# Performance work log

Measured on AMD Instinct MI355X. Metric: run time of the kernel, lower is better.

## Reference

```python
import jax, jax.numpy as jnp
import numpy as np

N_NODES = 50000
N_EDGES = 800000
NODE_DIM = 128
EDGE_DIM = 32
HIDDEN = 128
OUT_DIM = 128


def _linear_params(key, fan_in, fan_out):
    k1, k2 = jax.random.split(key)
    bound = 1.0 / np.sqrt(fan_in)
    W = jax.random.uniform(k1, (fan_in, fan_out), minval=-bound, maxval=bound, dtype=jnp.float32)
    b = jax.random.uniform(k2, (fan_out,), minval=-bound, maxval=bound, dtype=jnp.float32)
    return W, b


def setup_inputs() -> dict:
    key = jax.random.key(0)
    ks = jax.random.split(key, 7)
    h = jax.random.normal(ks[0], (N_NODES, NODE_DIM), dtype=jnp.float32)
    edge_index = jax.random.randint(ks[1], (2, N_EDGES), 0, N_NODES, dtype=jnp.int64)
    edge_attr = jax.random.normal(ks[2], (N_EDGES, EDGE_DIM), dtype=jnp.float32)
    We1, be1 = _linear_params(ks[3], 2 * NODE_DIM + EDGE_DIM, HIDDEN)
    We2, be2 = _linear_params(ks[4], HIDDEN, HIDDEN)
    Wh1, bh1 = _linear_params(ks[5], NODE_DIM + HIDDEN, HIDDEN)
    Wh2, bh2 = _linear_params(ks[6], HIDDEN, OUT_DIM)
    return {"h": h, "edge_index": edge_index, "edge_attr": edge_attr,
            "We1": We1, "be1": be1, "We2": We2, "be2": be2,
            "Wh1": Wh1, "bh1": bh1, "Wh2": Wh2, "bh2": bh2}


def _mlp(x, W1, b1, W2, b2):
    return jax.nn.relu(x @ W1 + b1) @ W2 + b2


def reference(h, edge_index, edge_attr, We1, be1, We2, be2, Wh1, bh1, Wh2, bh2):
    src = edge_index[0]
    dst = edge_index[1]
    # gather endpoint features and concat with edge attributes: [E, 2*D+De]
    edge_input = jnp.concatenate([h[src], h[dst], edge_attr], axis=-1)
    m_ij = _mlp(edge_input, We1, be1, We2, be2)  # [E, H]
    # scatter-add messages into destination nodes
    m_i = jax.ops.segment_sum(m_ij, dst, num_segments=h.shape[0])  # [N, H]
    node_input = jnp.concatenate([h, m_i], axis=-1)  # [N, D+H]
    h_next = _mlp(node_input, Wh1, bh1, Wh2, bh2)  # [N, out]
    return h_next
```

## Files before the change

### kernel.cpp

```cpp
#include <hip/hip_runtime.h>

#define E_TOTAL 800000
#define N_TOTAL 50000
#define NBINS   50176

typedef __attribute__((ext_vector_type(8))) short short8;
typedef __attribute__((ext_vector_type(4))) float floatx4;

__device__ __forceinline__ unsigned short f2bf(float f) {
    union { float f; unsigned u; } x; x.f = f;
    unsigned r = x.u + 0x7fff + ((x.u >> 16) & 1);
    return (unsigned short)(r >> 16);
}

__device__ __forceinline__ void gload_lds16(const void* g, void* l) {
    __builtin_amdgcn_global_load_lds(
        (const __attribute__((address_space(1))) void*)g,
        (__attribute__((address_space(3))) void*)l, 16, 0, 0);
}
__device__ __forceinline__ void gload_lds4(const void* g, void* l) {
    __builtin_amdgcn_global_load_lds(
        (const __attribute__((address_space(1))) void*)g,
        (__attribute__((address_space(3))) void*)l, 4, 0, 0);
}

__global__ __launch_bounds__(256)
void prep(const float* __restrict__ We1, const float* __restrict__ We2,
          const float* __restrict__ Wh1, const float* __restrict__ Wh2,
          unsigned short* __restrict__ W1t, unsigned short* __restrict__ W2t,
          unsigned short* __restrict__ Wh1t, unsigned short* __restrict__ Wh2t,
          const float* __restrict__ h, unsigned short* __restrict__ hbf,
          int do_cvt, int do_sort,
          float* __restrict__ mi, int* __restrict__ hist)
{
    const int b = blockIdx.x;
    const int tid = threadIdx.x;
    if (b < 400) {
        int t = b * 256 + tid;
        if (t < 36864) {
            W1t[(t & 127) * 288 + (t >> 7)] = f2bf(We1[t]);
        } else if (t < 53248) {
            t -= 36864;
            W2t[(t & 127) * 128 + (t >> 7)] = f2bf(We2[t]);
        } else if (t < 86016) {
            t -= 53248;
            Wh1t[(t & 127) * 256 + (t >> 7)] = f2bf(Wh1[t]);
        } else if (t < 102400) {
            t -= 86016;
            Wh2t[(t & 127) * 128 + (t >> 7)] = f2bf(Wh2[t]);
        }
    } else if (b < 6650) {
        const int t = (b - 400) * 256 + tid;
        ((float4*)mi)[t] = make_float4(0.f, 0.f, 0.f, 0.f);
    } else if (b < 9775) {
        if (do_cvt) {
            const int t = (b - 6650) * 256 + tid;
            const float4* h4 = (const float4*)h;
            float4 a = h4[(size_t)t * 2];
            float4 c = h4[(size_t)t * 2 + 1];
            short8 v = { (short)f2bf(a.x), (short)f2bf(a.y), (short)f2bf(a.z), (short)f2bf(a.w),
                         (short)f2bf(c.x), (short)f2bf(c.y), (short)f2bf(c.z), (short)f2bf(c.w) };
            *(short8*)(&hbf[(size_t)t * 8]) = v;
        }
    } else {
        if (do_sort) hist[(b - 9775) * 256 + tid] = 0;
    }
}

__global__ __launch_bounds__(256) void k_hist(const int* __restrict__ ei, int* __restrict__ hist) {
    const int t = blockIdx.x * 256 + threadIdx.x;
    atomicAdd(&hist[ei[E_TOTAL + t]], 1);
}
__global__ __launch_bounds__(256) void k_scan1(const int* __restrict__ hist, int* __restrict__ partial) {
    __shared__ int s[256];
    s[threadIdx.x] = hist[blockIdx.x * 256 + threadIdx.x];
    __syncthreads();
    for (int off = 128; off > 0; off >>= 1) {
        if (threadIdx.x < off) s[threadIdx.x] += s[threadIdx.x + off];
        __syncthreads();
    }
    if (threadIdx.x == 0) partial[blockIdx.x] = s[0];
}
__global__ __launch_bounds__(256)
void k_scan2(const int* __restrict__ partial, int* __restrict__ partialOff) {
    __shared__ int s[256];
    const int t = threadIdx.x;
    const int NP = NBINS / 256;
    const int v = (t < NP) ? partial[t] : 0;
    s[t] = v; __syncthreads();
    for (int off = 1; off < 256; off <<= 1) {
        int x = (t >= off) ? s[t - off] : 0;
        __syncthreads();
        s[t] += x;
        __syncthreads();
    }
    if (t < NP) partialOff[t] = s[t] - v;
}
__global__ __launch_bounds__(256)
void k_scan3(const int* __restrict__ hist, const int* __restrict__ partialOff,
             int* __restrict__ cursor) {
    __shared__ int s[256];
    const int t = threadIdx.x, g = blockIdx.x * 256 + t;
    const int v = hist[g];
    s[t] = v; __syncthreads();
    for (int off = 1; off < 256; off <<= 1) {
        int x = (t >= off) ? s[t - off] : 0;
        __syncthreads();
        s[t] += x;
        __syncthreads();
    }
    cursor[g] = partialOff[blockIdx.x] + s[t] - v;
}
__global__ __launch_bounds__(256)
void k_scatter(const int* __restrict__ ei, const float* __restrict__ ea,
               int* __restrict__ cursor,
               int* __restrict__ srcS, int* __restrict__ dstS,
               unsigned short* __restrict__ eabf) {
    const int t = blockIdx.x * 256 + threadIdx.x;
    const int src = ei[t];
    const int dst = ei[E_TOTAL + t];
    const int pos = atomicAdd(&cursor[dst], 1);
    srcS[pos] = src;
    dstS[pos] = dst;
    const float4* ea4 = (const float4*)ea;
    #pragma unroll
    for (int j = 0; j < 4; ++j) {
        float4 a = ea4[(size_t)t * 8 + j * 2];
        float4 b = ea4[(size_t)t * 8 + j * 2 + 1];
        short8 v = { (short)f2bf(a.x), (short)f2bf(a.y), (short)f2bf(a.z), (short)f2bf(a.w),
                     (short)f2bf(b.x), (short)f2bf(b.y), (short)f2bf(b.z), (short)f2bf(b.w) };
        *(short8*)(&eabf[(size_t)pos * 32 + j * 8]) = v;
    }
}

constexpr int XK = 296;
constexpr int HK = 136;
constexpr int NK = 264;
constexpr int FJ = 132;

#define MFMA8(A, B, C) { \
    C[0][0] = __builtin_amdgcn_mfma_f32_16x16x32_bf16(A[0], B[0], C[0][0], 0, 0, 0); \
    C[0][1] = __builtin_amdgcn_mfma_f32_16x16x32_bf16(A[0], B[1], C[0][1], 0, 0, 0); \
    C[1][0] = __builtin_amdgcn_mfma_f32_16x16x32_bf16(A[1], B[0], C[1][0], 0, 0, 0); \
    C[1][1] = __builtin_amdgcn_mfma_f32_16x16x32_bf16(A[1], B[1], C[1][1], 0, 0, 0); \
    C[2][0] = __builtin_amdgcn_mfma_f32_16x16x32_bf16(A[2], B[0], C[2][0], 0, 0, 0); \
    C[2][1] = __builtin_amdgcn_mfma_f32_16x16x32_bf16(A[2], B[1], C[2][1], 0, 0, 0); \
    C[3][0] = __builtin_amdgcn_mfma_f32_16x16x32_bf16(A[3], B[0], C[3][0], 0, 0, 0); \
    C[3][1] = __builtin_amdgcn_mfma_f32_16x16x32_bf16(A[3], B[1], C[3][1], 0, 0, 0); }

__global__ __launch_bounds__(256, 2)
void edge_mfma_sorted(const unsigned short* __restrict__ hbf,
                      const int* __restrict__ srcS,
                      const int* __restrict__ dstS,
                      const unsigned short* __restrict__ eabf,
                      const unsigned short* __restrict__ W1t,
                      const float* __restrict__ b1,
                      const unsigned short* __restrict__ W2t,
                      const float* __restrict__ b2,
                      float* __restrict__ mi)
{
    constexpr int NT = E_TOTAL / 64;
    constexpr int XH = 64 * 288;
    __shared__ alignas(16) unsigned short sMem[2 * XH + 768];
    int* idb = (int*)&sMem[2 * XH];

    const int tid  = threadIdx.x;
    const int lane = tid & 63;
    const int w    = tid >> 6;
    const int q    = lane >> 4;
    const int lr   = lane & 15;
    const int n0   = w * 32;
    const int q8   = q * 8;
    const int S    = (int)gridDim.x;

    const int w1b0 = (n0 + lr) * 288, w1b1 = (n0 + 16 + lr) * 288;
    const int w2b0 = (n0 + lr) * 128, w2b1 = (n0 + 16 + lr) * 128;
    const int h0 = lr * HK, h1 = (16 + lr) * HK, h2 = (32 + lr) * HK, h3 = (48 + lr) * HK;

    const float bias1[2] = { b1[n0 + lr], b1[n0 + 16 + lr] };
    const float bias2[2] = { b2[n0 + lr], b2[n0 + 16 + lr] };

    auto ID_DMA = [&](int tt, int k) {
        if (w == 0)      gload_lds4(srcS + tt * 64 + lane, &idb[k * 128]);
        else if (w == 1) gload_lds4(dstS + tt * 64 + lane, &idb[k * 128 + 64]);
    };

    auto X_DMA = [&](int tt, int bufS, int k) {
        const int* ids = &idb[k * 128];
        #pragma unroll
        for (int j = 0; j < 9; ++j) {
            const int tj = j * 256 + tid;
            const int e  = tj / 36;
            const int p  = tj - e * 36;
            const int c  = (p < 32) ? (p ^ (e & 15)) : p;
            const int node = ids[((c & 16) ? 64 : 0) + e];
            const char* gh = (const char*)hbf + (size_t)node * 256 + (size_t)(c & 15) * 16;
            const char* ge = (const char*)eabf + ((size_t)tt * 64 + e) * 64 + (size_t)(p - 32) * 16;
            const void* g  = (p < 32) ? (const void*)gh : (const void*)ge;
            gload_lds16(g, (void*)&sMem[bufS + j * 2048 + w * 512]);
        }
    };

#define LA1(KS, A) { \
    const int cs = ((KS) < 8) ? ((((KS) * 4 + q) ^ lr) * 8) : ((32 + q) * 8); \
    A[0] = *(const short8*)(&sX[( 0 + lr) * 288 + cs]); \
    A[1] = *(const short8*)(&sX[(16 + lr) * 288 + cs]); \
    A[2] = *(const short8*)(&sX[(32 + lr) * 288 + cs]); \
    A[3] = *(const short8*)(&sX[(48 + lr) * 288 + cs]); }
#define LB1(KS, B) { B[0] = *(const short8*)(&W1t[w1b0 + (KS) * 32 + q8]); \
                     B[1] = *(const short8*)(&W1t[w1b1 + (KS) * 32 + q8]); }
#define LA2(KS, A) { A[0] = *(const short8*)(&sX[h0 + (KS) * 32 + q8]); \
                     A[1] = *(const short8*)(&sX[h1 + (KS) * 32 + q8]); \
                     A[2] = *(const short8*)(&sX[h2 + (KS) * 32 + q8]); \
                     A[3] = *(const short8*)(&sX[h3 + (KS) * 32 + q8]); }
#define LB2(KS, B) { B[0] = *(const short8*)(&W2t[w2b0 + (KS) * 32 + q8]); \
                     B[1] = *(const short8*)(&W2t[w2b1 + (KS) * 32 + q8]); }

    int t  = blockIdx.x;
    int cur = 0, ib = 0;

    ID_DMA(t, 0);
    ID_DMA(t + S, 1);
    __syncthreads();
    X_DMA(t, 0, 0);
    __syncthreads();

    while (t < NT) {
        unsigned short* sX = &sMem[cur * XH];

        const int t2 = t + 2 * S;
        if (t2 < NT) ID_DMA(t2, (ib + 2) % 3);
        const int tn = t + S;
        if (tn < NT) X_DMA(tn, (cur ^ 1) * XH, (ib + 1) % 3);

        floatx4 acc[4][2];
        #pragma unroll
        for (int mt = 0; mt < 4; ++mt)
            #pragma unroll
            for (int nt = 0; nt < 2; ++nt)
                acc[mt][nt] = (floatx4){0.f, 0.f, 0.f, 0.f};
        {
            short8 aX[4], aY[4], bX[2], bY[2];
            LB1(0, bX); LB1(1, bY); LA1(0, aX);
            LA1(1, aY); MFMA8(aX, bX, acc); LB1(2, bX);
            LA1(2, aX); MFMA8(aY, bY, acc); LB1(3, bY);
            LA1(3, aY); MFMA8(aX, bX, acc); LB1(4, bX);
            LA1(4, aX); MFMA8(aY, bY, acc); LB1(5, bY);
            LA1(5, aY); MFMA8(aX, bX, acc); LB1(6, bX);
            LA1(6, aX); MFMA8(aY, bY, acc); LB1(7, bY);
            LA1(7, aY); MFMA8(aX, bX, acc); LB1(8, bX);
            LA1(8, aX); MFMA8(aY, bY, acc);
            MFMA8(aX, bX, acc);
        }
        __syncthreads();

        {
            #pragma unroll
            for (int mt = 0; mt < 4; ++mt)
                #pragma unroll
                for (int nt = 0; nt < 2; ++nt)
                    #pragma unroll
                    for (int r = 0; r < 4; ++r) {
                        float v = fmaxf(acc[mt][nt][r] + bias1[nt], 0.f);
                        sX[(mt * 16 + q * 4 + r) * HK + n0 + nt * 16 + lr] = f2bf(v);
                    }
        }
        __syncthreads();

        floatx4 acc2[4][2];
        #pragma unroll
        for (int mt = 0; mt < 4; ++mt)
            #pragma unroll
            for (int nt = 0; nt < 2; ++nt)
                acc2[mt][nt] = (floatx4){0.f, 0.f, 0.f, 0.f};
        {
            short8 aX[4], aY[4], bX[2], bY[2];
            LB2(0, bX); LB2(1, bY); LA2(0, aX);
            LA2(1, aY); MFMA8(aX, bX, acc2); LB2(2, bX);
            LA2(2, aX); MFMA8(aY, bY, acc2); LB2(3, bY);
            LA2(3, aY); MFMA8(aX, bX, acc2);
            MFMA8(aY, bY, acc2);
        }
        __syncthreads();

        float* sF = (float*)sX;
        {
            #pragma unroll
            for (int mt = 0; mt < 4; ++mt)
                #pragma unroll
                for (int nt = 0; nt < 2; ++nt)
                    #pragma unroll
                    for (int r = 0; r < 4; ++r)
                        sF[(mt * 16 + q * 4 + r) * FJ + n0 + nt * 16 + lr] =
                            acc2[mt][nt][r] + bias2[nt];
        }
        __syncthreads();

        {
            const int* idsDst = &idb[ib * 128 + 64];
            const int g  = tid >> 7;
            const int j  = tid & 127;
            const int r0 = g * 32;
            float sum = 0.f;
            for (int r = r0; r < r0 + 32; ++r) {
                sum += sF[r * FJ + j];
                const int dst = idsDst[r];
                if (r == r0 + 31 || idsDst[r + 1] != dst) {
                    atomicAdd(&mi[(size_t)dst * 128 + j], sum);
                    sum = 0.f;
                }
            }
        }
        __syncthreads();

        cur ^= 1;
        ib = (ib == 2) ? 0 : ib + 1;
        t = tn;
    }
#undef LA1
#undef LB1
#undef LA2
#undef LB2
}

template <bool PRECVT>
__global__ __launch_bounds__(256, 8)
void edge_mfma_flat(const float* __restrict__ h,
                    const unsigned short* __restrict__ hbf,
                    const int* __restrict__ ei,
                    const float* __restrict__ ea,
                    const unsigned short* __restrict__ W1t,
                    const float* __restrict__ b1,
                    const unsigned short* __restrict__ W2t,
                    const float* __restrict__ b2,
                    float* __restrict__ mi)
{
    __shared__ unsigned short sMem[32 * XK];
    __shared__ int sDst[32];

    const int tid = threadIdx.x;
    const int e0  = blockIdx.x * 32;
    if (tid < 32) sDst[tid] = ei[E_TOTAL + e0 + tid];

    const float4* h4   = (const float4*)h;
    const short8* hbf8 = (const short8*)hbf;
    const float4* ea4  = (const float4*)ea;
    #pragma unroll
    for (int it = 0; it < 5; ++it) {
        const int idx = tid + it * 256;
        const int e  = idx / 40;
        const int c  = idx - e * 40;
        const int ge = e0 + e;
        if (c < 32) {
            const int node = (c < 16) ? ei[ge] : ei[E_TOTAL + ge];
            const int cc = c & 15;
            short8 v;
            if (PRECVT) {
                v = hbf8[(size_t)node * 16 + cc];
            } else {
                float4 x = h4[(size_t)node * 32 + cc * 2];
                float4 y = h4[(size_t)node * 32 + cc * 2 + 1];
                v = (short8){ (short)f2bf(x.x), (short)f2bf(x.y), (short)f2bf(x.z), (short)f2bf(x.w),
                              (short)f2bf(y.x), (short)f2bf(y.y), (short)f2bf(y.z), (short)f2bf(y.w) };
            }
            *(short8*)(&sMem[e * XK + c * 8]) = v;
        } else {
            float4 x = ea4[(size_t)ge * 8 + (c - 32)];
            unsigned short* p = &sMem[e * XK + 128 + c * 4];
            p[0] = f2bf(x.x); p[1] = f2bf(x.y); p[2] = f2bf(x.z); p[3] = f2bf(x.w);
        }
    }
    __syncthreads();

    const int lane = tid & 63;
    const int w    = tid >> 6;
    const int q    = lane >> 4;
    const int lr   = lane & 15;
    const int n0   = w * 32;

    floatx4 acc[2][2];
    #pragma unroll
    for (int mt = 0; mt < 2; ++mt)
        #pragma unroll
        for (int nt = 0; nt < 2; ++nt)
            acc[mt][nt] = (floatx4){0.f, 0.f, 0.f, 0.f};
    #pragma unroll
    for (int ks = 0; ks < 9; ++ks) {
        const int kb = ks * 32 + q * 8;
        short8 a[2], b[2];
        #pragma unroll
        for (int mt = 0; mt < 2; ++mt)
            a[mt] = *(const short8*)(&sMem[(mt * 16 + lr) * XK + kb]);
        #pragma unroll
        for (int nt = 0; nt < 2; ++nt)
            b[nt] = *(const short8*)(&W1t[(n0 + nt * 16 + lr) * 288 + kb]);
        #pragma unroll
        for (int mt = 0; mt < 2; ++mt)
            #pragma unroll
            for (int nt = 0; nt < 2; ++nt)
                acc[mt][nt] = __builtin_amdgcn_mfma_f32_16x16x32_bf16(
                    a[mt], b[nt], acc[mt][nt], 0, 0, 0);
    }
    __syncthreads();
    {
        float bias[2] = { b1[n0 + lr], b1[n0 + 16 + lr] };
        #pragma unroll
        for (int mt = 0; mt < 2; ++mt)
            #pragma unroll
            for (int nt = 0; nt < 2; ++nt)
                #pragma unroll
                for (int r = 0; r < 4; ++r) {
                    float v = fmaxf(acc[mt][nt][r] + bias[nt], 0.f);
                    sMem[(mt * 16 + q * 4 + r) * HK + n0 + nt * 16 + lr] = f2bf(v);
                }
    }
    __syncthreads();
    floatx4 acc2[2][2];
    #pragma unroll
    for (int mt = 0; mt < 2; ++mt)
        #pragma unroll
        for (int nt = 0; nt < 2; ++nt)
            acc2[mt][nt] = (floatx4){0.f, 0.f, 0.f, 0.f};
    #pragma unroll
    for (int ks = 0; ks < 4; ++ks) {
        const int kb = ks * 32 + q * 8;
        short8 a[2], b[2];
        #pragma unroll
        for (int mt = 0; mt < 2; ++mt)
            a[mt] = *(const short8*)(&sMem[(mt * 16 + lr) * HK + kb]);
        #pragma unroll
        for (int nt = 0; nt < 2; ++nt)
            b[nt] = *(const short8*)(&W2t[(n0 + nt * 16 + lr) * 128 + kb]);
        #pragma unroll
        for (int mt = 0; mt < 2; ++mt)
            #pragma unroll
            for (int nt = 0; nt < 2; ++nt)
                acc2[mt][nt] = __builtin_amdgcn_mfma_f32_16x16x32_bf16(
                    a[mt], b[nt], acc2[mt][nt], 0, 0, 0);
    }
    {
        float bias[2] = { b2[n0 + lr], b2[n0 + 16 + lr] };
        #pragma unroll
        for (int mt = 0; mt < 2; ++mt)
            #pragma unroll
            for (int r = 0; r < 4; ++r) {
                const int m   = mt * 16 + q * 4 + r;
                const int dst = sDst[m];
                float* row = &mi[(size_t)dst * 128];
                #pragma unroll
                for (int nt = 0; nt < 2; ++nt)
                    atomicAdd(&row[n0 + nt * 16 + lr], acc2[mt][nt][r] + bias[nt]);
            }
    }
}

template <bool USEHBF>
__global__ __launch_bounds__(256, 8)
void node_mfma(const float* __restrict__ h,
               const unsigned short* __restrict__ hbf,
               const float* __restrict__ mi,
               const unsigned short* __restrict__ W1t,
               const float* __restrict__ b1,
               const unsigned short* __restrict__ W2t,
               const float* __restrict__ b2,
               float* __restrict__ out)
{
    __shared__ unsigned short sMem[32 * NK];

    const int tid = threadIdx.x;
    const int g0  = blockIdx.x * 32;

    const float4* h4   = (const float4*)h;
    const short8* hbf8 = (const short8*)hbf;
    const float4* mi4  = (const float4*)mi;
    if (USEHBF) {
        #pragma unroll
        for (int it = 0; it < 2; ++it) {
            const int idx = tid + it * 256;
            const int n  = idx >> 4;
            const int c  = idx & 15;
            const int gn = g0 + n;
            short8 v = (short8){0,0,0,0,0,0,0,0};
            if (gn < N_TOTAL) v = hbf8[(size_t)gn * 16 + c];
            *(short8*)(&sMem[n * NK + c * 8]) = v;
        }
        #pragma unroll
        for (int it = 0; it < 4; ++it) {
            const int idx = tid + it * 256;
            const int n  = idx >> 5;
            const int c  = idx & 31;
            const int gn = g0 + n;
            float4 v = make_float4(0.f, 0.f, 0.f, 0.f);
            if (gn < N_TOTAL) v = mi4[(size_t)gn * 32 + c];
            unsigned short* p = &sMem[n * NK + 128 + c * 4];
            p[0] = f2bf(v.x); p[1] = f2bf(v.y); p[2] = f2bf(v.z); p[3] = f2bf(v.w);
        }
    } else {
        #pragma unroll
        for (int it = 0; it < 8; ++it) {
            const int idx = tid + it * 256;
            const int n  = idx >> 6;
            const int c  = idx & 63;
            const int gn = g0 + n;
            float4 v = make_float4(0.f, 0.f, 0.f, 0.f);
            if (gn < N_TOTAL)
                v = (c < 32) ? h4[(size_t)gn * 32 + c] : mi4[(size_t)gn * 32 + (c - 32)];
            unsigned short* p = &sMem[n * NK + c * 4];
            p[0] = f2bf(v.x); p[1] = f2bf(v.y); p[2] = f2bf(v.z); p[3] = f2bf(v.w);
        }
    }
    __syncthreads();

    const int lane = tid & 63;
    const int w    = tid >> 6;
    const int q    = lane >> 4;
    const int lr   = lane & 15;
    const int n0   = w * 32;

    floatx4 acc[2][2];
    #pragma unroll
    for (int mt = 0; mt < 2; ++mt)
        #pragma unroll
        for (int nt = 0; nt < 2; ++nt)
            acc[mt][nt] = (floatx4){0.f, 0.f, 0.f, 0.f};
    #pragma unroll
    for (int ks = 0; ks < 8; ++ks) {
        const int kb = ks * 32 + q * 8;
        short8 a[2], b[2];
        #pragma unroll
        for (int mt = 0; mt < 2; ++mt)
            a[mt] = *(const short8*)(&sMem[(mt * 16 + lr) * NK + kb]);
        #pragma unroll
        for (int nt = 0; nt < 2; ++nt)
            b[nt] = *(const short8*)(&W1t[(n0 + nt * 16 + lr) * 256 + kb]);
        #pragma unroll
        for (int mt = 0; mt < 2; ++mt)
            #pragma unroll
            for (int nt = 0; nt < 2; ++nt)
                acc[mt][nt] = __builtin_amdgcn_mfma_f32_16x16x32_bf16(
                    a[mt], b[nt], acc[mt][nt], 0, 0, 0);
    }
    __syncthreads();
    {
        float bias[2] = { b1[n0 + lr], b1[n0 + 16 + lr] };
        #pragma unroll
        for (int mt = 0; mt < 2; ++mt)
            #pragma unroll
            for (int nt = 0; nt < 2; ++nt)
                #pragma unroll
                for (int r = 0; r < 4; ++r) {
                    float v = fmaxf(acc[mt][nt][r] + bias[nt], 0.f);
                    sMem[(mt * 16 + q * 4 + r) * HK + n0 + nt * 16 + lr] = f2bf(v);
                }
    }
    __syncthreads();
    floatx4 acc2[2][2];
    #pragma unroll
    for (int mt = 0; mt < 2; ++mt)
        #pragma unroll
        for (int nt = 0; nt < 2; ++nt)
            acc2[mt][nt] = (floatx4){0.f, 0.f, 0.f, 0.f};
    #pragma unroll
    for (int ks = 0; ks < 4; ++ks) {
        const int kb = ks * 32 + q * 8;
        short8 a[2], b[2];
        #pragma unroll
        for (int mt = 0; mt < 2; ++mt)
            a[mt] = *(const short8*)(&sMem[(mt * 16 + lr) * HK + kb]);
        #pragma unroll
        for (int nt = 0; nt < 2; ++nt)
            b[nt] = *(const short8*)(&W2t[(n0 + nt * 16 + lr) * 128 + kb]);
        #pragma unroll
        for (int mt = 0; mt < 2; ++mt)
            #pragma unroll
            for (int nt = 0; nt < 2; ++nt)
                acc2[mt][nt] = __builtin_amdgcn_mfma_f32_16x16x32_bf16(
                    a[mt], b[nt], acc2[mt][nt], 0, 0, 0);
    }
    {
        float bias[2] = { b2[n0 + lr], b2[n0 + 16 + lr] };
        #pragma unroll
        for (int mt = 0; mt < 2; ++mt)
            #pragma unroll
            for (int r = 0; r < 4; ++r) {
                const int gm = g0 + mt * 16 + q * 4 + r;
                if (gm < N_TOTAL) {
                    #pragma unroll
                    for (int nt = 0; nt < 2; ++nt)
                        out[(size_t)gm * 128 + n0 + nt * 16 + lr] =
                            acc2[mt][nt][r] + bias[nt];
                }
            }
    }
}

extern "C" void kernel_launch(void* const* d_in, const int* in_sizes, int n_in,
                              void* d_out, int out_size, void* d_ws, size_t ws_size,
                              hipStream_t stream) {
    const float* h   = (const float*)d_in[0];
    const int*   ei  = (const int*)d_in[1];
    const float* ea  = (const float*)d_in[2];
    const float* We1 = (const float*)d_in[3];
    const float* be1 = (const float*)d_in[4];
    const float* We2 = (const float*)d_in[5];
    const float* be2 = (const float*)d_in[6];
    const float* Wh1 = (const float*)d_in[7];
    const float* bh1 = (const float*)d_in[8];
    const float* Wh2 = (const float*)d_in[9];
    const float* bh2 = (const float*)d_in[10];
    float* out = (float*)d_out;

    const size_t szMi   = (size_t)N_TOTAL * 128 * sizeof(float);
    const size_t szW1t  = 128 * 288 * 2;
    const size_t szW2t  = 128 * 128 * 2;
    const size_t szWh1t = 128 * 256 * 2;
    const size_t szWh2t = 128 * 128 * 2;
    const size_t szHbf  = (size_t)N_TOTAL * 128 * 2;
    const size_t szIds  = (size_t)E_TOTAL * 4;
    const size_t szEabf = (size_t)E_TOTAL * 32 * 2;
    const size_t szHist = (size_t)NBINS * 4;

    const size_t offW1t  = szMi;
    const size_t offW2t  = offW1t + szW1t;
    const size_t offWh1t = offW2t + szW2t;
    const size_t offWh2t = offWh1t + szWh1t;
    const size_t offHbf  = offWh2t + szWh2t;
    const size_t offSrc  = offHbf + szHbf;
    const size_t offDst  = offSrc + szIds;
    const size_t offEabf = offDst + szIds;
    const size_t offHist = offEabf + szEabf;
    const size_t offCur  = offHist + szHist;
    const size_t offP1   = offCur + szHist;
    const size_t offP2   = offP1 + 1024;
    const size_t needFull = offP2 + 1024;
    const size_t needCvt  = offSrc;

    char* wsb = (char*)d_ws;
    float* mi = (float*)wsb;
    unsigned short* W1t  = (unsigned short*)(wsb + offW1t);
    unsigned short* W2t  = (unsigned short*)(wsb + offW2t);
    unsigned short* Wh1t = (unsigned short*)(wsb + offWh1t);
    unsigned short* Wh2t = (unsigned short*)(wsb + offWh2t);
    unsigned short* hbf  = (unsigned short*)(wsb + offHbf);
    int* srcS    = (int*)(wsb + offSrc);
    int* dstS    = (int*)(wsb + offDst);
    unsigned short* eabf = (unsigned short*)(wsb + offEabf);
    int* hist    = (int*)(wsb + offHist);
    int* cursor  = (int*)(wsb + offCur);
    int* partial = (int*)(wsb + offP1);
    int* poff    = (int*)(wsb + offP2);

    const int full   = (ws_size >= needFull) ? 1 : 0;
    const int do_cvt = (ws_size >= needCvt + szHbf) ? 1 : 0;

    prep<<<9971, 256, 0, stream>>>(We1, We2, Wh1, Wh2, W1t, W2t, Wh1t, Wh2t,
                                   h, hbf, do_cvt, full, mi, hist);

    if (full) {
        k_hist<<<E_TOTAL / 256, 256, 0, stream>>>(ei, hist);
        k_scan1<<<NBINS / 256, 256, 0, stream>>>(hist, partial);
        k_scan2<<<1, 256, 0, stream>>>(partial, poff);
        k_scan3<<<NBINS / 256, 256, 0, stream>>>(hist, poff, cursor);
        k_scatter<<<E_TOTAL / 256, 256, 0, stream>>>(ei, ea, cursor, srcS, dstS, eabf);
        edge_mfma_sorted<<<512, 256, 0, stream>>>(
            hbf, srcS, dstS, eabf, W1t, be1, W2t, be2, mi);
        node_mfma<true><<<(N_TOTAL + 31) / 32, 256, 0, stream>>>(
            h, hbf, mi, Wh1t, bh1, Wh2t, bh2, out);
    } else if (do_cvt) {
        edge_mfma_flat<true><<<E_TOTAL / 32, 256, 0, stream>>>(
            h, hbf, ei, ea, W1t, be1, W2t, be2, mi);
        node_mfma<true><<<(N_TOTAL + 31) / 32, 256, 0, stream>>>(
            h, hbf, mi, Wh1t, bh1, Wh2t, bh2, out);
    } else {
        edge_mfma_flat<false><<<E_TOTAL / 32, 256, 0, stream>>>(
            h, nullptr, ei, ea, W1t, be1, W2t, be2, mi);
        node_mfma<false><<<(N_TOTAL + 31) / 32, 256, 0, stream>>>(
            h, nullptr, mi, Wh1t, bh1, Wh2t, bh2, out);
    }
    (void)in_sizes; (void)n_in; (void)out_size;
}
```

Before: 443.4 us.

## Fuse sort kernels into one cooperative launch, remap edge blocks, raise MFMA priority

Merges the histogram, three scan kernels and scatter into one cooperative kernel of 512 blocks separated by grid syncs, removing four launches and their gaps. The sorted edge kernel now remaps block IDs so consecutive blocks are spread across groups of eight, and raises wave priority around the MFMA loops with s_setprio. The segmented scatter-add loop is unrolled into two interleaved 16-row chains. Grid syncs add their own cost, and the cooperative launch needs all 512 blocks resident at once.

Result: slower. 624.5 us (+40.8%).

```diff
diff --git a/kernel.cpp b/kernel.cpp
--- a/kernel.cpp
+++ b/kernel.cpp
@@ -1,4 +1,5 @@
 #include <hip/hip_runtime.h>
+#include <hip/hip_cooperative_groups.h>
 
 #define E_TOTAL 800000
 #define N_TOTAL 50000
@@ -67,69 +68,64 @@
     }
 }
 
-__global__ __launch_bounds__(256) void k_hist(const int* __restrict__ ei, int* __restrict__ hist) {
-    const int t = blockIdx.x * 256 + threadIdx.x;
-    atomicAdd(&hist[ei[E_TOTAL + t]], 1);
-}
-__global__ __launch_bounds__(256) void k_scan1(const int* __restrict__ hist, int* __restrict__ partial) {
+__global__ __launch_bounds__(256)
+void k_sort(const int* __restrict__ ei, const float* __restrict__ ea,
+            int* __restrict__ hist, int* __restrict__ cursor,
+            int* __restrict__ srcS, int* __restrict__ dstS,
+            unsigned short* __restrict__ eabf, int* __restrict__ partial)
+{
+    namespace cg = cooperative_groups;
+    cg::grid_group grid = cg::this_grid();
+    const int tid = threadIdx.x, bid = blockIdx.x;
+    const int gthreads = (int)gridDim.x * 256;
+
+    for (int t = bid * 256 + tid; t < E_TOTAL; t += gthreads)
+        atomicAdd(&hist[ei[E_TOTAL + t]], 1);
+    grid.sync();
+
     __shared__ int s[256];
-    s[threadIdx.x] = hist[blockIdx.x * 256 + threadIdx.x];
-    __syncthreads();
-    for (int off = 128; off > 0; off >>= 1) {
-        if (threadIdx.x < off) s[threadIdx.x] += s[threadIdx.x + off];
-        __syncthreads();
-    }
-    if (threadIdx.x == 0) partial[blockIdx.x] = s[0];
-}
-__global__ __launch_bounds__(256)
-void k_scan2(const int* __restrict__ partial, int* __restrict__ partialOff) {
-    __shared__ int s[256];
-    const int t = threadIdx.x;
-    const int NP = NBINS / 256;
-    const int v = (t < NP) ? partial[t] : 0;
-    s[t] = v; __syncthreads();
-    for (int off = 1; off < 256; off <<= 1) {
-        int x = (t >= off) ? s[t - off] : 0;
-        __syncthreads();
-        s[t] += x;
-        __syncthreads();
-    }
-    if (t < NP) partialOff[t] = s[t] - v;
-}
-__global__ __launch_bounds__(256)
-void k_scan3(const int* __restrict__ hist, const int* __restrict__ partialOff,
-             int* __restrict__ cursor) {
-    __shared__ int s[256];
-    const int t = threadIdx.x, g = blockIdx.x * 256 + t;
-    const int v = hist[g];
-    s[t] = v; __syncthreads();
-    for (int off = 1; off < 256; off <<= 1) {
-        int x = (t >= off) ? s[t - off] : 0;
-        __syncthreads();
-        s[t] += x;
-        __syncthreads();
-    }
-    cursor[g] = partialOff[blockIdx.x] + s[t] - v;
-}
-__global__ __launch_bounds__(256)
-void k_scatter(const int* __restrict__ ei, const float* __restrict__ ea,
-               int* __restrict__ cursor,
-               int* __restrict__ srcS, int* __restrict__ dstS,
-               unsigned short* __restrict__ eabf) {
-    const int t = blockIdx.x * 256 + threadIdx.x;
-    const int src = ei[t];
-    const int dst = ei[E_TOTAL + t];
-    const int pos = atomicAdd(&cursor[dst], 1);
-    srcS[pos] = src;
-    dstS[pos] = dst;
+    int local_ex = 0, myv = 0;
+    if (bid < NBINS / 256) {
+        const int g = bid * 256 + tid;
+        myv = hist[g];
+        s[tid] = myv; __syncthreads();
+        for (int off = 1; off < 256; off <<= 1) {
+            int x = (tid >= off) ? s[tid - off] : 0;
+            __syncthreads(); s[tid] += x; __syncthreads();
+        }
+        if (tid == 255) partial[bid] = s[255];
+        local_ex = s[tid] - myv;
+    }
+    grid.sync();
+
+    if (bid < NBINS / 256) {
+        const int NP = NBINS / 256;
+        int pv = (tid < NP) ? partial[tid] : 0;
+        s[tid] = pv; __syncthreads();
+        for (int off = 1; off < 256; off <<= 1) {
+            int x = (tid >= off) ? s[tid - off] : 0;
+            __syncthreads(); s[tid] += x; __syncthreads();
+        }
+        const int blockOff = (bid == 0) ? 0 : s[bid - 1];
+        cursor[bid * 256 + tid] = blockOff + local_ex;
+    }
+    grid.sync();
+
     const float4* ea4 = (const float4*)ea;
-    #pragma unroll
-    for (int j = 0; j < 4; ++j) {
-        float4 a = ea4[(size_t)t * 8 + j * 2];
-        float4 b = ea4[(size_t)t * 8 + j * 2 + 1];
-        short8 v = { (short)f2bf(a.x), (short)f2bf(a.y), (short)f2bf(a.z), (short)f2bf(a.w),
-                     (short)f2bf(b.x), (short)f2bf(b.y), (short)f2bf(b.z), (short)f2bf(b.w) };
-        *(short8*)(&eabf[(size_t)pos * 32 + j * 8]) = v;
+    for (int t = bid * 256 + tid; t < E_TOTAL; t += gthreads) {
+        const int src = ei[t];
+        const int dst = ei[E_TOTAL + t];
+        const int pos = atomicAdd(&cursor[dst], 1);
+        srcS[pos] = src;
+        dstS[pos] = dst;
+        #pragma unroll
+        for (int j = 0; j < 4; ++j) {
+            float4 a = ea4[(size_t)t * 8 + j * 2];
+            float4 b = ea4[(size_t)t * 8 + j * 2 + 1];
+            short8 v = { (short)f2bf(a.x), (short)f2bf(a.y), (short)f2bf(a.z), (short)f2bf(a.w),
+                         (short)f2bf(b.x), (short)f2bf(b.y), (short)f2bf(b.z), (short)f2bf(b.w) };
+            *(short8*)(&eabf[(size_t)pos * 32 + j * 8]) = v;
+        }
     }
 }
 
@@ -172,6 +168,7 @@
     const int n0   = w * 32;
     const int q8   = q * 8;
     const int S    = (int)gridDim.x;
+    const int b0   = ((int)blockIdx.x & 7) * 64 + ((int)blockIdx.x >> 3);
 
     const int w1b0 = (n0 + lr) * 288, w1b1 = (n0 + 16 + lr) * 288;
     const int w2b0 = (n0 + lr) * 128, w2b1 = (n0 + 16 + lr) * 128;
@@ -216,7 +213,7 @@
 #define LB2(KS, B) { B[0] = *(const short8*)(&W2t[w2b0 + (KS) * 32 + q8]); \
                      B[1] = *(const short8*)(&W2t[w2b1 + (KS) * 32 + q8]); }
 
-    int t  = blockIdx.x;
+    int t  = b0;
     int cur = 0, ib = 0;
 
     ID_DMA(t, 0);
@@ -239,6 +236,7 @@
             #pragma unroll
             for (int nt = 0; nt < 2; ++nt)
                 acc[mt][nt] = (floatx4){0.f, 0.f, 0.f, 0.f};
+        __builtin_amdgcn_s_setprio(1);
         {
             short8 aX[4], aY[4], bX[2], bY[2];
             LB1(0, bX); LB1(1, bY); LA1(0, aX);
@@ -252,6 +250,7 @@
             LA1(8, aX); MFMA8(aY, bY, acc);
             MFMA8(aX, bX, acc);
         }
+        __builtin_amdgcn_s_setprio(0);
         __syncthreads();
 
         {
@@ -273,6 +272,7 @@
             #pragma unroll
             for (int nt = 0; nt < 2; ++nt)
                 acc2[mt][nt] = (floatx4){0.f, 0.f, 0.f, 0.f};
+        __builtin_amdgcn_s_setprio(1);
         {
             short8 aX[4], aY[4], bX[2], bY[2];
             LB2(0, bX); LB2(1, bY); LA2(0, aX);
@@ -281,6 +281,7 @@
             LA2(3, aY); MFMA8(aX, bX, acc2);
             MFMA8(aY, bY, acc2);
         }
+        __builtin_amdgcn_s_setprio(0);
         __syncthreads();
 
         float* sF = (float*)sX;
@@ -298,16 +299,21 @@
 
         {
             const int* idsDst = &idb[ib * 128 + 64];
-            const int g  = tid >> 7;
+            const int gq = tid >> 7;
             const int j  = tid & 127;
-            const int r0 = g * 32;
-            float sum = 0.f;
-            for (int r = r0; r < r0 + 32; ++r) {
-                sum += sF[r * FJ + j];
-                const int dst = idsDst[r];
-                if (r == r0 + 31 || idsDst[r + 1] != dst) {
-                    atomicAdd(&mi[(size_t)dst * 128 + j], sum);
-                    sum = 0.f;
+            const int r0 = gq * 32;
+            float sum0 = 0.f, sum1 = 0.f;
+            #pragma unroll
+            for (int k = 0; k < 16; ++k) {
+                const int ra = r0 + k, rb = r0 + 16 + k;
+                sum0 += sF[ra * FJ + j];
+                sum1 += sF[rb * FJ + j];
+                const int da = idsDst[ra], db = idsDst[rb];
+                if (k == 15 || idsDst[ra + 1] != da) {
+                    atomicAdd(&mi[(size_t)da * 128 + j], sum0); sum0 = 0.f;
+                }
+                if (k == 15 || idsDst[rb + 1] != db) {
+                    atomicAdd(&mi[(size_t)db * 128 + j], sum1); sum1 = 0.f;
                 }
             }
         }
@@ -648,7 +654,6 @@
     int* hist    = (int*)(wsb + offHist);
     int* cursor  = (int*)(wsb + offCur);
     int* partial = (int*)(wsb + offP1);
-    int* poff    = (int*)(wsb + offP2);
 
     const int full   = (ws_size >= needFull) ? 1 : 0;
     const int do_cvt = (ws_size >= needCvt + szHbf) ? 1 : 0;
@@ -657,11 +662,10 @@
                                    h, hbf, do_cvt, full, mi, hist);
 
     if (full) {
-        k_hist<<<E_TOTAL / 256, 256, 0, stream>>>(ei, hist);
-        k_scan1<<<NBINS / 256, 256, 0, stream>>>(hist, partial);
-        k_scan2<<<1, 256, 0, stream>>>(partial, poff);
-        k_scan3<<<NBINS / 256, 256, 0, stream>>>(hist, poff, cursor);
-        k_scatter<<<E_TOTAL / 256, 256, 0, stream>>>(ei, ea, cursor, srcS, dstS, eabf);
+        void* ksArgs[] = { (void*)&ei, (void*)&ea, (void*)&hist, (void*)&cursor,
+                           (void*)&srcS, (void*)&dstS, (void*)&eabf, (void*)&partial };
+        hipLaunchCooperativeKernel((const void*)k_sort, dim3(512), dim3(256),
+                                   ksArgs, 0, stream);
         edge_mfma_sorted<<<512, 256, 0, stream>>>(
             hbf, srcS, dstS, eabf, W1t, be1, W2t, be2, mi);
         node_mfma<true><<<(N_TOTAL + 31) / 32, 256, 0, stream>>>(
```

## Remap tile order per XCD, raise MFMA wave priority, split scatter into two chains

Applied to the files above, without the earlier changes.

The starting tile index is remapped so consecutive block IDs are spread in an XCD-aware pattern (blockIdx&7)*64 + blockIdx>>3. s_setprio raises wave priority around the MFMA sections so matrix work is favoured over the DMA and scatter phases of other waves. The scatter-add loop is unrolled into two independent 16-row segment-sum chains to add instruction-level parallelism, at the cost of up to one extra atomic per column. The remap assumes a grid of 512 blocks; any other grid size would produce wrong or out-of-range tile indices.

Result: no change. 445.0 us (+0.4%).

```diff
diff --git a/kernel.cpp b/kernel.cpp
--- a/kernel.cpp
+++ b/kernel.cpp
@@ -172,6 +172,7 @@
     const int n0   = w * 32;
     const int q8   = q * 8;
     const int S    = (int)gridDim.x;
+    const int b0   = ((int)blockIdx.x & 7) * 64 + ((int)blockIdx.x >> 3);
 
     const int w1b0 = (n0 + lr) * 288, w1b1 = (n0 + 16 + lr) * 288;
     const int w2b0 = (n0 + lr) * 128, w2b1 = (n0 + 16 + lr) * 128;
@@ -216,7 +217,7 @@
 #define LB2(KS, B) { B[0] = *(const short8*)(&W2t[w2b0 + (KS) * 32 + q8]); \
                      B[1] = *(const short8*)(&W2t[w2b1 + (KS) * 32 + q8]); }
 
-    int t  = blockIdx.x;
+    int t  = b0;
     int cur = 0, ib = 0;
 
     ID_DMA(t, 0);
@@ -239,6 +240,7 @@
             #pragma unroll
             for (int nt = 0; nt < 2; ++nt)
                 acc[mt][nt] = (floatx4){0.f, 0.f, 0.f, 0.f};
+        __builtin_amdgcn_s_setprio(1);
         {
             short8 aX[4], aY[4], bX[2], bY[2];
             LB1(0, bX); LB1(1, bY); LA1(0, aX);
@@ -252,6 +254,7 @@
             LA1(8, aX); MFMA8(aY, bY, acc);
             MFMA8(aX, bX, acc);
         }
+        __builtin_amdgcn_s_setprio(0);
         __syncthreads();
 
         {
@@ -273,6 +276,7 @@
             #pragma unroll
             for (int nt = 0; nt < 2; ++nt)
                 acc2[mt][nt] = (floatx4){0.f, 0.f, 0.f, 0.f};
+        __builtin_amdgcn_s_setprio(1);
         {
             short8 aX[4], aY[4], bX[2], bY[2];
             LB2(0, bX); LB2(1, bY); LA2(0, aX);
@@ -281,6 +285,7 @@
             LA2(3, aY); MFMA8(aX, bX, acc2);
             MFMA8(aY, bY, acc2);
         }
+        __builtin_amdgcn_s_setprio(0);
         __syncthreads();
 
         float* sF = (float*)sX;
@@ -298,16 +303,21 @@
 
         {
             const int* idsDst = &idb[ib * 128 + 64];
-            const int g  = tid >> 7;
+            const int gq = tid >> 7;
             const int j  = tid & 127;
-            const int r0 = g * 32;
-            float sum = 0.f;
-            for (int r = r0; r < r0 + 32; ++r) {
-                sum += sF[r * FJ + j];
-                const int dst = idsDst[r];
-                if (r == r0 + 31 || idsDst[r + 1] != dst) {
-                    atomicAdd(&mi[(size_t)dst * 128 + j], sum);
-                    sum = 0.f;
+            const int r0 = gq * 32;
+            float sum0 = 0.f, sum1 = 0.f;
+            #pragma unroll
+            for (int k = 0; k < 16; ++k) {
+                const int ra = r0 + k, rb = r0 + 16 + k;
+                sum0 += sF[ra * FJ + j];
+                sum1 += sF[rb * FJ + j];
+                const int da = idsDst[ra], db = idsDst[rb];
+                if (k == 15 || idsDst[ra + 1] != da) {
+                    atomicAdd(&mi[(size_t)da * 128 + j], sum0); sum0 = 0.f;
+                }
+                if (k == 15 || idsDst[rb + 1] != db) {
+                    atomicAdd(&mi[(size_t)db * 128 + j], sum1); sum1 = 0.f;
                 }
             }
         }
```
